# Kernel tuning notes

Measured on AMD Instinct MI355X. Metric: run time of the kernel, lower is better.

Reference implementation:

```python
import jax, jax.numpy as jnp
import numpy as np

N = 128            # cache entries selected per ray (init arg n)
M = 3 * N          # cache rows
B = 65536          # rays in batch
NUM_SAMPLES = 256  # total samples per ray; inner sampler supplies NUM_SAMPLES - N


def _unit(k, shape):
    v = jax.random.normal(k, shape, dtype=jnp.float32)
    return v / jnp.linalg.norm(v, axis=-1, keepdims=True)


def setup_inputs() -> dict:
    key = jax.random.key(0)
    k0, k1, k2, k3, k4, k5 = jax.random.split(key, 6)
    cache_dirs = _unit(k0, (M, 3))
    cache_mip = jax.random.uniform(k1, (M, 1), dtype=jnp.float32)
    cache_bright = jax.random.uniform(k2, (M, 1), dtype=jnp.float32)
    cache = jnp.concatenate([cache_dirs, cache_mip, cache_bright], axis=1)  # (M,5)
    refdirs = _unit(k3, (B, 3))
    normal = _unit(k4, (B, 3))
    samp_rays = _unit(k5, (B, NUM_SAMPLES - N, 3))
    samp_mipval = jax.random.uniform(jax.random.fold_in(k5, 1), (B, NUM_SAMPLES - N), dtype=jnp.float32)
    return {"cache": cache, "refdirs": refdirs, "normal": normal,
            "samp_rays": samp_rays, "samp_mipval": samp_mipval}


def reference(cache, refdirs, normal, samp_rays, samp_mipval):
    # BrightnessSampler.sample with cache_init=True (n = N cache rays appended).
    cache_dirs = cache[:, :3]      # (M,3)
    cache_mip = cache[:, 3]        # (M,)
    # hemisphere test and directional similarity against every cached ray
    hemi = jnp.einsum('bd,md->bm', normal, cache_dirs)    # (B,M)
    sim = jnp.einsum('bd,md->bm', refdirs, cache_dirs)    # (B,M)
    score = jnp.where(hemi > 0, -sim, jnp.float32(0.0))   # (B,M)
    # torch: inds = argsort(score, dim=1) < n ; boolean-mask gather in original
    # position order. Replicate: keep original positions j where order[b,j] < N.
    order = jnp.argsort(score, axis=1)                    # (B,M)
    mask = order < N
    pos = jnp.where(mask, jnp.arange(M)[None, :], M)
    sel_pos = jnp.sort(pos, axis=1)[:, :N]                # (B,N) ascending original positions
    sel_rays = cache_dirs[sel_pos]                        # (B,N,3)
    sel_mipval = cache_mip[sel_pos]                       # (B,N)
    rays = jnp.concatenate([samp_rays, sel_rays], axis=1)       # (B,NUM_SAMPLES,3)
    mipval = jnp.concatenate([samp_mipval, sel_mipval], axis=1)  # (B,NUM_SAMPLES)
    return rays, mipval
```

## Files before the change

kernel.cpp:

```cpp
#include <hip/hip_runtime.h>

#define NCACHE 384

__device__ __forceinline__ unsigned int sortable_bits(float f) {
    unsigned int u = __float_as_uint(f);
    return (u & 0x80000000u) ? ~u : (u | 0x80000000u);
}


#define JLT4(Q)                                                     \
    "v_cmp_lt_u32 vcc, " Q ", %[k0]\n\t"                            \
    "v_cmp_lt_u32 %[sA], " Q ", %[k1]\n\t"                          \
    "v_cmp_lt_u32 %[sB], " Q ", %[k2]\n\t"                          \
    "v_cmp_lt_u32 %[sC], " Q ", %[k3]\n\t"                          \
    "v_addc_co_u32 %[r0], vcc, 0, %[r0], vcc\n\t"                   \
    "v_addc_co_u32 %[r1], %[sA], 0, %[r1], %[sA]\n\t"               \
    "v_addc_co_u32 %[r2], %[sB], 0, %[r2], %[sB]\n\t"               \
    "v_addc_co_u32 %[r3], %[sC], 0, %[r3], %[sC]\n\t"

#define JOWN(Q, JOS, KO, RO, O1, K1, R1, O2, K2, R2, O3, K3, R3)    \
    "v_cmp_lt_u32 vcc, " Q ", %[" KO "]\n\t"                        \
    "v_cmp_" O1 "_u32 %[sA], " Q ", %[" K1 "]\n\t"                  \
    "v_cmp_" O2 "_u32 %[sB], " Q ", %[" K2 "]\n\t"                  \
    "v_cmp_" O3 "_u32 %[sC], " Q ", %[" K3 "]\n\t"                  \
    "v_addc_co_u32 %[" RO "], vcc, 0, %[" RO "], vcc\n\t"           \
    "v_addc_co_u32 %[" R1 "], %[sA], 0, %[" R1 "], %[sA]\n\t"       \
    "v_addc_co_u32 %[" R2 "], %[sB], 0, %[" R2 "], %[sB]\n\t"       \
    "v_addc_co_u32 %[" R3 "], %[sC], 0, %[" R3 "], %[sC]\n\t"       \
    "v_cmp_eq_u32 vcc, " Q ", %[" KO "]\n\t"                        \
    "v_bfe_u32 %[t], %[M], " JOS ", 1\n\t"                          \
    "v_cndmask_b32 %[t], 0, %[t], vcc\n\t"                          \
    "v_add_u32 %[" RO "], %[t], %[" RO "]\n\t"

#define ITER_OWN(QV, J0, J1, J2, J3, KO, RO, O1, K1, R1, O2, K2, R2, O3, K3, R3) \
    do {                                                            \
        asm(JOWN("%[a]", J0, KO, RO, O1, K1, R1, O2, K2, R2, O3, K3, R3) \
            JOWN("%[b]", J1, KO, RO, O1, K1, R1, O2, K2, R2, O3, K3, R3) \
            JOWN("%[c]", J2, KO, RO, O1, K1, R1, O2, K2, R2, O3, K3, R3) \
            JOWN("%[d]", J3, KO, RO, O1, K1, R1, O2, K2, R2, O3, K3, R3) \
            : [r0]"+v"(r0), [r1]"+v"(r1), [r2]"+v"(r2), [r3]"+v"(r3), \
              [t]"=&v"(t), [sA]"=&s"(scA), [sB]"=&s"(scB), [sC]"=&s"(scC) \
            : [a]"v"(QV.x), [b]"v"(QV.y), [c]"v"(QV.z), [d]"v"(QV.w), \
              [k0]"v"(vk0), [k1]"v"(vk1), [k2]"v"(vk2), [k3]"v"(vk3), \
              [M]"v"(Mmask)                                         \
            : "vcc");                                               \
    } while (0)

#define OWN8(KB, KO, RO, O1, K1, R1, O2, K2, R2, O3, K3, R3)                                  \
    { uint4 q = vq[(KB)*8 + 0]; ITER_OWN(q, "0","1","2","3",     KO,RO,O1,K1,R1,O2,K2,R2,O3,K3,R3); } \
    { uint4 q = vq[(KB)*8 + 1]; ITER_OWN(q, "4","5","6","7",     KO,RO,O1,K1,R1,O2,K2,R2,O3,K3,R3); } \
    { uint4 q = vq[(KB)*8 + 2]; ITER_OWN(q, "8","9","10","11",   KO,RO,O1,K1,R1,O2,K2,R2,O3,K3,R3); } \
    { uint4 q = vq[(KB)*8 + 3]; ITER_OWN(q, "12","13","14","15", KO,RO,O1,K1,R1,O2,K2,R2,O3,K3,R3); } \
    { uint4 q = vq[(KB)*8 + 4]; ITER_OWN(q, "16","17","18","19", KO,RO,O1,K1,R1,O2,K2,R2,O3,K3,R3); } \
    { uint4 q = vq[(KB)*8 + 5]; ITER_OWN(q, "20","21","22","23", KO,RO,O1,K1,R1,O2,K2,R2,O3,K3,R3); } \
    { uint4 q = vq[(KB)*8 + 6]; ITER_OWN(q, "24","25","26","27", KO,RO,O1,K1,R1,O2,K2,R2,O3,K3,R3); } \
    { uint4 q = vq[(KB)*8 + 7]; ITER_OWN(q, "28","29","30","31", KO,RO,O1,K1,R1,O2,K2,R2,O3,K3,R3); }

__global__ __launch_bounds__(256, 8) void fused_kernel(
    const float*  __restrict__ cache,
    const float*  __restrict__ refdirs,
    const float*  __restrict__ normal,
    const float4* __restrict__ samp_rays4,
    const float4* __restrict__ samp_mip4,
    float* __restrict__ out, int B)
{
#pragma clang fp contract(off)
    __shared__ __align__(16) float4 scache[NCACHE];
    __shared__ __align__(16) unsigned int vals[8][NCACHE];
    __shared__ unsigned int bitmap[8][12];

    const int tid  = threadIdx.x;
    const int wave = tid >> 6;
    const int lane = tid & 63;
    const int h    = lane >> 5;
    const int l5   = lane & 31;
    const int vidx = wave * 2 + h;
    const int myb  = blockIdx.x * 8 + vidx;

    const int bbase = blockIdx.x * 8;
    const int ia = tid, ib = tid + 256, ic = tid + 512, id = tid + 768;
    const int ba = bbase + (ia >> 7), oa = ia & 127;
    const int bbb = bbase + (ib >> 7), ob = ib & 127;
    const int bc = bbase + (ic >> 7), oc = ic & 127;
    const int bd = bbase + (id >> 7), od = id & 127;
    const float4 ca = (oa < 96) ? samp_rays4[(size_t)ba * 96 + oa]
                                : samp_mip4[(size_t)ba * 32 + (oa - 96)];
    const float4 cb = (ob < 96) ? samp_rays4[(size_t)bbb * 96 + ob]
                                : samp_mip4[(size_t)bbb * 32 + (ob - 96)];
    const float4 cc = (oc < 96) ? samp_rays4[(size_t)bc * 96 + oc]
                                : samp_mip4[(size_t)bc * 32 + (oc - 96)];
    const float4 cd = (od < 96) ? samp_rays4[(size_t)bd * 96 + od]
                                : samp_mip4[(size_t)bd * 32 + (od - 96)];

    for (int m = tid; m < NCACHE; m += 256) {
        scache[m] = make_float4(cache[m * 5 + 0], cache[m * 5 + 1],
                                cache[m * 5 + 2], cache[m * 5 + 3]);
    }
    if (tid < 96) (&bitmap[0][0])[tid] = 0u;

    const float nx = normal[myb * 3 + 0], ny = normal[myb * 3 + 1], nz = normal[myb * 3 + 2];
    const float rx = refdirs[myb * 3 + 0], ry = refdirs[myb * 3 + 1], rz = refdirs[myb * 3 + 2];

    __syncthreads();

    unsigned int vk0 = 0, vk1 = 0, vk2 = 0, vk3 = 0;
#pragma unroll
    for (int c = 0; c < 12; ++c) {
        const int m = c * 32 + l5;
        const float4 d = scache[m];
        float hemi = __builtin_fmaf(nz, d.z, __builtin_fmaf(ny, d.y, nx * d.x));
        float sim  = __builtin_fmaf(rz, d.z, __builtin_fmaf(ry, d.y, rx * d.x));
        float val  = (hemi > 0.0f) ? -sim : 0.0f;
        val = val + 0.0f;
        const unsigned int sv = sortable_bits(val);
        vals[vidx][m] = sv;
        if (c == 0) vk0 = sv;
        if (c == 1) vk1 = sv;
        if (c == 2) vk2 = sv;
        if (c == 3) vk3 = sv;
    }

    const uint4* vq = (const uint4*)&vals[vidx][0];
    const unsigned int Mmask = (1u << l5) - 1u;
    unsigned int r0 = 0, r1 = 0, r2 = 0, r3 = 0;
    unsigned int t;
    unsigned long long scA, scB, scC;

    OWN8(0, "k0", "r0", "le", "k1", "r1", "le", "k2", "r2", "le", "k3", "r3");
    OWN8(1, "k1", "r1", "lt", "k0", "r0", "le", "k2", "r2", "le", "k3", "r3");
    OWN8(2, "k2", "r2", "lt", "k0", "r0", "lt", "k1", "r1", "le", "k3", "r3");
    OWN8(3, "k3", "r3", "lt", "k0", "r0", "lt", "k1", "r1", "lt", "k2", "r2");

#pragma unroll 8
    for (int i = 32; i < 96; ++i) {
        const uint4 q = vq[i];
        asm(JLT4("%[a]") JLT4("%[b]") JLT4("%[c]") JLT4("%[d]")
            : [r0]"+v"(r0), [r1]"+v"(r1), [r2]"+v"(r2), [r3]"+v"(r3),
              [sA]"=&s"(scA), [sB]"=&s"(scB), [sC]"=&s"(scC)
            : [a]"v"(q.x), [b]"v"(q.y), [c]"v"(q.z), [d]"v"(q.w),
              [k0]"v"(vk0), [k1]"v"(vk1), [k2]"v"(vk2), [k3]"v"(vk3)
            : "vcc");
    }

    atomicOr(&bitmap[vidx][r0 >> 5], 1u << (r0 & 31));
    atomicOr(&bitmap[vidx][r1 >> 5], 1u << (r1 & 31));
    atomicOr(&bitmap[vidx][r2 >> 5], 1u << (r2 & 31));
    atomicOr(&bitmap[vidx][r3 >> 5], 1u << (r3 & 31));

    float* out_rays = out;
    float* out_mip  = out + (size_t)B * 768;

#pragma unroll
    for (int c = 0; c < 4; ++c) {
        const unsigned int r = (c == 0) ? r0 : (c == 1) ? r1 : (c == 2) ? r2 : r3;
        const int wi = (int)(r >> 5);
        int s = __popc(bitmap[vidx][wi] & ((1u << (r & 31)) - 1u));
        for (int w = 0; w < wi; ++w) s += __popc(bitmap[vidx][w]);
        const float4 g = scache[r];
        const size_t rb = (size_t)myb * 768 + 384 + (size_t)s * 3;
        out_rays[rb + 0] = g.x;
        out_rays[rb + 1] = g.y;
        out_rays[rb + 2] = g.z;
        out_mip[(size_t)myb * 256 + 128 + s] = g.w;
    }

    float4* out4     = (float4*)out;
    float4* out_mip4 = (float4*)(out + (size_t)B * 768);
    if (oa < 96) out4[(size_t)ba * 192 + oa] = ca;
    else         out_mip4[(size_t)ba * 64 + (oa - 96)] = ca;
    if (ob < 96) out4[(size_t)bbb * 192 + ob] = cb;
    else         out_mip4[(size_t)bbb * 64 + (ob - 96)] = cb;
    if (oc < 96) out4[(size_t)bc * 192 + oc] = cc;
    else         out_mip4[(size_t)bc * 64 + (oc - 96)] = cc;
    if (od < 96) out4[(size_t)bd * 192 + od] = cd;
    else         out_mip4[(size_t)bd * 64 + (od - 96)] = cd;
}

extern "C" void kernel_launch(void* const* d_in, const int* in_sizes, int n_in,
                              void* d_out, int out_size, void* d_ws, size_t ws_size,
                              hipStream_t stream) {
    const float* cache       = (const float*)d_in[0];
    const float* refdirs     = (const float*)d_in[1];
    const float* normal      = (const float*)d_in[2];
    const float* samp_rays   = (const float*)d_in[3];
    const float* samp_mipval = (const float*)d_in[4];
    float* out = (float*)d_out;

    const int B = in_sizes[1] / 3;

    fused_kernel<<<B / 8, 256, 0, stream>>>(cache, refdirs, normal,
                                            (const float4*)samp_rays,
                                            (const float4*)samp_mipval,
                                            out, B);
}
```

Measured before the change: 231.9 us.

## Replace carry-based rank counting with sub/shift arithmetic and stream sample copy early

Rank counting over the 384 scores no longer uses v_cmp into SGPR masks plus v_addc. Each comparison is now a VGPR subtract and arithmetic shift, with the sign added into or subtracted from the counter. Constant offsets applied at the end fix up the less-or-equal counts, and ties use a min/bfi sequence. The pass-through copy of the inner samples now goes straight from global loads to stores at kernel start instead of being held in registers to the end. Launch bounds drop to 4 waves per EU and the inner unroll shrinks to 4. This trades SGPR and carry-chain dependencies for more VALU instructions per comparison. It relies on score bit patterns differing by less than 2^31.

```diff
diff --git a/kernel.cpp b/kernel.cpp
--- a/kernel.cpp
+++ b/kernel.cpp
@@ -8,55 +8,64 @@
 }
 
 
-#define JLT4(Q)                                                     \
-    "v_cmp_lt_u32 vcc, " Q ", %[k0]\n\t"                            \
-    "v_cmp_lt_u32 %[sA], " Q ", %[k1]\n\t"                          \
-    "v_cmp_lt_u32 %[sB], " Q ", %[k2]\n\t"                          \
-    "v_cmp_lt_u32 %[sC], " Q ", %[k3]\n\t"                          \
-    "v_addc_co_u32 %[r0], vcc, 0, %[r0], vcc\n\t"                   \
-    "v_addc_co_u32 %[r1], %[sA], 0, %[r1], %[sA]\n\t"               \
-    "v_addc_co_u32 %[r2], %[sB], 0, %[r2], %[sB]\n\t"               \
-    "v_addc_co_u32 %[r3], %[sC], 0, %[r3], %[sC]\n\t"
+#define P_LT(J, K, D) "v_sub_u32 " D ", " J ", " K "\n\t"
+#define P_LE(J, K, D) "v_sub_u32 " D ", " K ", " J "\n\t"
+#define SH(D)         "v_ashrrev_i32 " D ", 31, " D "\n\t"
+#define A_LT(R, D)    "v_sub_u32 " R ", " R ", " D "\n\t"
+#define A_LE(R, D)    "v_add_u32 " R ", " R ", " D "\n\t"
 
-#define JOWN(Q, JOS, KO, RO, O1, K1, R1, O2, K2, R2, O3, K3, R3)    \
-    "v_cmp_lt_u32 vcc, " Q ", %[" KO "]\n\t"                        \
-    "v_cmp_" O1 "_u32 %[sA], " Q ", %[" K1 "]\n\t"                  \
-    "v_cmp_" O2 "_u32 %[sB], " Q ", %[" K2 "]\n\t"                  \
-    "v_cmp_" O3 "_u32 %[sC], " Q ", %[" K3 "]\n\t"                  \
-    "v_addc_co_u32 %[" RO "], vcc, 0, %[" RO "], vcc\n\t"           \
-    "v_addc_co_u32 %[" R1 "], %[sA], 0, %[" R1 "], %[sA]\n\t"       \
-    "v_addc_co_u32 %[" R2 "], %[sB], 0, %[" R2 "], %[sB]\n\t"       \
-    "v_addc_co_u32 %[" R3 "], %[sC], 0, %[" R3 "], %[sC]\n\t"       \
-    "v_cmp_eq_u32 vcc, " Q ", %[" KO "]\n\t"                        \
-    "v_bfe_u32 %[t], %[M], " JOS ", 1\n\t"                          \
-    "v_cndmask_b32 %[t], 0, %[t], vcc\n\t"                          \
-    "v_add_u32 %[" RO "], %[t], %[" RO "]\n\t"
+#define J2(Ja, Jb, P0, A0, P1, A1, P2, A2, P3, A3)              \
+    P0(Ja, "%[k0]", "%[d0]") P1(Ja, "%[k1]", "%[d1]")           \
+    P2(Ja, "%[k2]", "%[d2]") P3(Ja, "%[k3]", "%[d3]")           \
+    P0(Jb, "%[k0]", "%[d4]") P1(Jb, "%[k1]", "%[d5]")           \
+    P2(Jb, "%[k2]", "%[d6]") P3(Jb, "%[k3]", "%[d7]")           \
+    SH("%[d0]") SH("%[d1]") SH("%[d2]") SH("%[d3]")             \
+    SH("%[d4]") SH("%[d5]") SH("%[d6]") SH("%[d7]")             \
+    A0("%[r0]", "%[d0]") A1("%[r1]", "%[d1]")                   \
+    A2("%[r2]", "%[d2]") A3("%[r3]", "%[d3]")                   \
+    A0("%[r0]", "%[d4]") A1("%[r1]", "%[d5]")                   \
+    A2("%[r2]", "%[d6]") A3("%[r3]", "%[d7]")
 
-#define ITER_OWN(QV, J0, J1, J2, J3, KO, RO, O1, K1, R1, O2, K2, R2, O3, K3, R3) \
-    do {                                                            \
-        asm(JOWN("%[a]", J0, KO, RO, O1, K1, R1, O2, K2, R2, O3, K3, R3) \
-            JOWN("%[b]", J1, KO, RO, O1, K1, R1, O2, K2, R2, O3, K3, R3) \
-            JOWN("%[c]", J2, KO, RO, O1, K1, R1, O2, K2, R2, O3, K3, R3) \
-            JOWN("%[d]", J3, KO, RO, O1, K1, R1, O2, K2, R2, O3, K3, R3) \
-            : [r0]"+v"(r0), [r1]"+v"(r1), [r2]"+v"(r2), [r3]"+v"(r3), \
-              [t]"=&v"(t), [sA]"=&s"(scA), [sB]"=&s"(scB), [sC]"=&s"(scC) \
-            : [a]"v"(QV.x), [b]"v"(QV.y), [c]"v"(QV.z), [d]"v"(QV.w), \
-              [k0]"v"(vk0), [k1]"v"(vk1), [k2]"v"(vk2), [k3]"v"(vk3), \
-              [M]"v"(Mmask)                                         \
-            : "vcc");                                               \
+#define TIE2(Ja, JOa, Jb, JOb, K, R)                            \
+    "v_xor_b32 %[x0], " Ja ", " K "\n\t"                        \
+    "v_xor_b32 %[x1], " Jb ", " K "\n\t"                        \
+    "v_min_u32 %[x0], 1, %[x0]\n\t"                             \
+    "v_min_u32 %[x1], 1, %[x1]\n\t"                             \
+    "v_bfe_u32 %[x2], %[M], " JOa ", 1\n\t"                     \
+    "v_bfe_u32 %[x3], %[M], " JOb ", 1\n\t"                     \
+    "v_bfi_b32 %[x0], %[x0], 0, %[x2]\n\t"                      \
+    "v_bfi_b32 %[x1], %[x1], 0, %[x3]\n\t"                      \
+    "v_add_u32 " R ", " R ", %[x0]\n\t"                         \
+    "v_add_u32 " R ", " R ", %[x1]\n\t"
+
+#define ASM_IO                                                          \
+    : [r0]"+v"(r0), [r1]"+v"(r1), [r2]"+v"(r2), [r3]"+v"(r3),           \
+      [d0]"=&v"(d0), [d1]"=&v"(d1), [d2]"=&v"(d2), [d3]"=&v"(d3),       \
+      [d4]"=&v"(d4), [d5]"=&v"(d5), [d6]"=&v"(d6), [d7]"=&v"(d7),       \
+      [x0]"=&v"(x0), [x1]"=&v"(x1), [x2]"=&v"(x2), [x3]"=&v"(x3)        \
+    : [a]"v"(q.x), [b]"v"(q.y), [c]"v"(q.z), [d]"v"(q.w),               \
+      [k0]"v"(vk0), [k1]"v"(vk1), [k2]"v"(vk2), [k3]"v"(vk3), [M]"v"(Mmask)
+
+#define OWN_U4(Q, JO0, JO1, JO2, JO3, P0,A0,P1,A1,P2,A2,P3,A3, KO, RO)  \
+    do { const uint4 q = (Q);                                           \
+        asm(J2("%[a]", "%[b]", P0,A0,P1,A1,P2,A2,P3,A3)                 \
+            J2("%[c]", "%[d]", P0,A0,P1,A1,P2,A2,P3,A3)                 \
+            TIE2("%[a]", JO0, "%[b]", JO1, KO, RO)                      \
+            TIE2("%[c]", JO2, "%[d]", JO3, KO, RO)                      \
+            ASM_IO);                                                    \
     } while (0)
 
-#define OWN8(KB, KO, RO, O1, K1, R1, O2, K2, R2, O3, K3, R3)                                  \
-    { uint4 q = vq[(KB)*8 + 0]; ITER_OWN(q, "0","1","2","3",     KO,RO,O1,K1,R1,O2,K2,R2,O3,K3,R3); } \
-    { uint4 q = vq[(KB)*8 + 1]; ITER_OWN(q, "4","5","6","7",     KO,RO,O1,K1,R1,O2,K2,R2,O3,K3,R3); } \
-    { uint4 q = vq[(KB)*8 + 2]; ITER_OWN(q, "8","9","10","11",   KO,RO,O1,K1,R1,O2,K2,R2,O3,K3,R3); } \
-    { uint4 q = vq[(KB)*8 + 3]; ITER_OWN(q, "12","13","14","15", KO,RO,O1,K1,R1,O2,K2,R2,O3,K3,R3); } \
-    { uint4 q = vq[(KB)*8 + 4]; ITER_OWN(q, "16","17","18","19", KO,RO,O1,K1,R1,O2,K2,R2,O3,K3,R3); } \
-    { uint4 q = vq[(KB)*8 + 5]; ITER_OWN(q, "20","21","22","23", KO,RO,O1,K1,R1,O2,K2,R2,O3,K3,R3); } \
-    { uint4 q = vq[(KB)*8 + 6]; ITER_OWN(q, "24","25","26","27", KO,RO,O1,K1,R1,O2,K2,R2,O3,K3,R3); } \
-    { uint4 q = vq[(KB)*8 + 7]; ITER_OWN(q, "28","29","30","31", KO,RO,O1,K1,R1,O2,K2,R2,O3,K3,R3); }
+#define OWN_BLOCK(C, P0,A0,P1,A1,P2,A2,P3,A3, KO, RO)                               \
+    OWN_U4(vq[(C)*8+0], "0","1","2","3",     P0,A0,P1,A1,P2,A2,P3,A3, KO, RO);      \
+    OWN_U4(vq[(C)*8+1], "4","5","6","7",     P0,A0,P1,A1,P2,A2,P3,A3, KO, RO);      \
+    OWN_U4(vq[(C)*8+2], "8","9","10","11",   P0,A0,P1,A1,P2,A2,P3,A3, KO, RO);      \
+    OWN_U4(vq[(C)*8+3], "12","13","14","15", P0,A0,P1,A1,P2,A2,P3,A3, KO, RO);      \
+    OWN_U4(vq[(C)*8+4], "16","17","18","19", P0,A0,P1,A1,P2,A2,P3,A3, KO, RO);      \
+    OWN_U4(vq[(C)*8+5], "20","21","22","23", P0,A0,P1,A1,P2,A2,P3,A3, KO, RO);      \
+    OWN_U4(vq[(C)*8+6], "24","25","26","27", P0,A0,P1,A1,P2,A2,P3,A3, KO, RO);      \
+    OWN_U4(vq[(C)*8+7], "28","29","30","31", P0,A0,P1,A1,P2,A2,P3,A3, KO, RO);
 
-__global__ __launch_bounds__(256, 8) void fused_kernel(
+__global__ __launch_bounds__(256, 4) void fused_kernel(
     const float*  __restrict__ cache,
     const float*  __restrict__ refdirs,
     const float*  __restrict__ normal,
@@ -77,20 +86,21 @@
     const int vidx = wave * 2 + h;
     const int myb  = blockIdx.x * 8 + vidx;
 
-    const int bbase = blockIdx.x * 8;
-    const int ia = tid, ib = tid + 256, ic = tid + 512, id = tid + 768;
-    const int ba = bbase + (ia >> 7), oa = ia & 127;
-    const int bbb = bbase + (ib >> 7), ob = ib & 127;
-    const int bc = bbase + (ic >> 7), oc = ic & 127;
-    const int bd = bbase + (id >> 7), od = id & 127;
-    const float4 ca = (oa < 96) ? samp_rays4[(size_t)ba * 96 + oa]
-                                : samp_mip4[(size_t)ba * 32 + (oa - 96)];
-    const float4 cb = (ob < 96) ? samp_rays4[(size_t)bbb * 96 + ob]
-                                : samp_mip4[(size_t)bbb * 32 + (ob - 96)];
-    const float4 cc = (oc < 96) ? samp_rays4[(size_t)bc * 96 + oc]
-                                : samp_mip4[(size_t)bc * 32 + (oc - 96)];
-    const float4 cd = (od < 96) ? samp_rays4[(size_t)bd * 96 + od]
-                                : samp_mip4[(size_t)bd * 32 + (od - 96)];
+    {
+        float4* out4     = (float4*)out;
+        float4* out_mip4 = (float4*)(out + (size_t)B * 768);
+        const int bbase = blockIdx.x * 8;
+#pragma unroll
+        for (int s = 0; s < 4; ++s) {
+            const int i  = tid + s * 256;
+            const int bb = bbase + (i >> 7), off = i & 127;
+            if (off < 96) {
+                out4[(size_t)bb * 192 + off] = samp_rays4[(size_t)bb * 96 + off];
+            } else {
+                out_mip4[(size_t)bb * 64 + (off - 96)] = samp_mip4[(size_t)bb * 32 + (off - 96)];
+            }
+        }
+    }
 
     for (int m = tid; m < NCACHE; m += 256) {
         scache[m] = make_float4(cache[m * 5 + 0], cache[m * 5 + 1],
@@ -123,24 +133,22 @@
     const uint4* vq = (const uint4*)&vals[vidx][0];
     const unsigned int Mmask = (1u << l5) - 1u;
     unsigned int r0 = 0, r1 = 0, r2 = 0, r3 = 0;
-    unsigned int t;
-    unsigned long long scA, scB, scC;
+    unsigned int d0, d1, d2, d3, d4, d5, d6, d7, x0, x1, x2, x3;
 
-    OWN8(0, "k0", "r0", "le", "k1", "r1", "le", "k2", "r2", "le", "k3", "r3");
-    OWN8(1, "k1", "r1", "lt", "k0", "r0", "le", "k2", "r2", "le", "k3", "r3");
-    OWN8(2, "k2", "r2", "lt", "k0", "r0", "lt", "k1", "r1", "le", "k3", "r3");
-    OWN8(3, "k3", "r3", "lt", "k0", "r0", "lt", "k1", "r1", "lt", "k2", "r2");
+    OWN_BLOCK(0, P_LT,A_LT, P_LE,A_LE, P_LE,A_LE, P_LE,A_LE, "%[k0]", "%[r0]");
+    OWN_BLOCK(1, P_LT,A_LT, P_LT,A_LT, P_LE,A_LE, P_LE,A_LE, "%[k1]", "%[r1]");
+    OWN_BLOCK(2, P_LT,A_LT, P_LT,A_LT, P_LT,A_LT, P_LE,A_LE, "%[k2]", "%[r2]");
+    OWN_BLOCK(3, P_LT,A_LT, P_LT,A_LT, P_LT,A_LT, P_LT,A_LT, "%[k3]", "%[r3]");
 
-#pragma unroll 8
+#pragma unroll 4
     for (int i = 32; i < 96; ++i) {
         const uint4 q = vq[i];
-        asm(JLT4("%[a]") JLT4("%[b]") JLT4("%[c]") JLT4("%[d]")
-            : [r0]"+v"(r0), [r1]"+v"(r1), [r2]"+v"(r2), [r3]"+v"(r3),
-              [sA]"=&s"(scA), [sB]"=&s"(scB), [sC]"=&s"(scC)
-            : [a]"v"(q.x), [b]"v"(q.y), [c]"v"(q.z), [d]"v"(q.w),
-              [k0]"v"(vk0), [k1]"v"(vk1), [k2]"v"(vk2), [k3]"v"(vk3)
-            : "vcc");
+        asm(J2("%[a]", "%[b]", P_LT,A_LT, P_LT,A_LT, P_LT,A_LT, P_LT,A_LT)
+            J2("%[c]", "%[d]", P_LT,A_LT, P_LT,A_LT, P_LT,A_LT, P_LT,A_LT)
+            ASM_IO);
     }
+
+    r1 += 32u; r2 += 64u; r3 += 96u;
 
     atomicOr(&bitmap[vidx][r0 >> 5], 1u << (r0 & 31));
     atomicOr(&bitmap[vidx][r1 >> 5], 1u << (r1 & 31));
@@ -163,17 +171,6 @@
         out_rays[rb + 2] = g.z;
         out_mip[(size_t)myb * 256 + 128 + s] = g.w;
     }
-
-    float4* out4     = (float4*)out;
-    float4* out_mip4 = (float4*)(out + (size_t)B * 768);
-    if (oa < 96) out4[(size_t)ba * 192 + oa] = ca;
-    else         out_mip4[(size_t)ba * 64 + (oa - 96)] = ca;
-    if (ob < 96) out4[(size_t)bbb * 192 + ob] = cb;
-    else         out_mip4[(size_t)bbb * 64 + (ob - 96)] = cb;
-    if (oc < 96) out4[(size_t)bc * 192 + oc] = cc;
-    else         out_mip4[(size_t)bc * 64 + (oc - 96)] = cc;
-    if (od < 96) out4[(size_t)bd * 192 + od] = cd;
-    else         out_mip4[(size_t)bd * 64 + (od - 96)] = cd;
 }
 
 extern "C" void kernel_launch(void* const* d_in, const int* in_sizes, int n_in,
```

After: 285.9 us. 23.3% more time.
